# Performance work log

Measured on AMD Instinct MI355X. Metric: run time of the kernel, lower is better.

Reference implementation:

```python
import jax, jax.numpy as jnp
import numpy as np


def _get_pairs(top_k_centers):
    """Returns (p0, p1) int32 arrays of shape [B, S]: for each object a, the
    IoU-best partner a', ordered so the larger-L1 box comes first (as in source)."""
    cx, cy, h, w = jnp.split(top_k_centers, 4, axis=-1)  # [B,S,1] each, cxcyhw
    box = jnp.concatenate([cx - 0.5 * w, cy - 0.5 * h, cx + 0.5 * w, cy + 0.5 * h], axis=-1)  # [B,S,4] xyxy
    S = box.shape[1]
    b1 = box[:, :, None, :]  # [B,S,1,4]
    b2 = box[:, None, :, :]  # [B,1,S,4]
    inter_mins = jnp.maximum(b1[..., :2], b2[..., :2])
    inter_maxs = jnp.maximum(b1[..., 2:], b2[..., 2:])  # NOTE: source uses maximum here (kept faithful)
    inter_wh = jnp.clip(inter_maxs - inter_mins, 0.0)
    inter_area = inter_wh[..., 0] * inter_wh[..., 1]  # [B,S,S]
    area = (box[..., 2] - box[..., 0]) * (box[..., 3] - box[..., 1])  # [B,S]
    union = area[:, :, None] + area[:, None, :] - inter_area
    iou = inter_area / union - jnp.eye(S, dtype=inter_area.dtype)
    partner = jnp.argmax(iou, axis=-1)  # [B,S] int
    self_idx = jnp.broadcast_to(jnp.arange(S), partner.shape)
    l1 = jnp.abs(box[..., 2] - box[..., 0]) + jnp.abs(box[..., 3] - box[..., 1])  # [B,S]
    l1_partner = jnp.take_along_axis(l1, partner, axis=-1)
    keep = l1 >= l1_partner  # larger-L1 element goes first
    p0 = jnp.where(keep, self_idx, partner)
    p1 = jnp.where(keep, partner, self_idx)
    return p0, p1


def _gather_pair(a2, p):
    # a2: [B,H,S,S]; p: [B,S]. out[b,h,a,c] = a2[b,h,p[b,a],p[b,c]]
    rows = jnp.take_along_axis(a2, p[:, None, :, None], axis=2)
    return jnp.take_along_axis(rows, p[:, None, None, :], axis=3)


def setup_inputs() -> dict:
    key = jax.random.key(0)
    kq, kk, kv, kc = jax.random.split(key, 4)
    B, H, S, D = 8, 8, 1024, 64
    return {
        "query": jax.random.normal(kq, (B, H, S, D), dtype=jnp.float32),
        "key": jax.random.normal(kk, (B, H, S, D), dtype=jnp.float32),
        "value": jax.random.normal(kv, (B, H, S, D), dtype=jnp.float32),
        "top_k_centers": jax.random.uniform(kc, (B, S, 4), dtype=jnp.float32),
    }


def reference(query, key, value, top_k_centers):
    B, H, S, D = query.shape
    p0, p1 = _get_pairs(top_k_centers)
    # A2(a,b) = <q_{pi_a}, k_{pi_b}> + <q_{pi_a'}, k_{pi_b'}>
    a2 = jnp.einsum('bhqd,bhkd->bhqk', query, key)  # [B,H,S,S]
    scores = (_gather_pair(a2, p0) + _gather_pair(a2, p1)) * (1.0 / np.sqrt(2.0 * D))
    attn = jax.nn.softmax(scores, axis=-1)
    o2 = jnp.einsum('bhqk,bhkd->bhqd', attn, value)  # [B,H,S,D]
    return o2.transpose(0, 2, 1, 3).reshape(B, S, H * D)
```

## Files before the change

### kernel.cpp

```cpp
#include <hip/hip_runtime.h>
#include <hip/hip_bf16.h>

#define B_ 8
#define H_ 8
#define S_ 1024
#define D_ 64
#define KT 32
#define NSTEP 16

typedef float f32x16 __attribute__((ext_vector_type(16)));
typedef short s16x8 __attribute__((ext_vector_type(8)));
typedef unsigned int u32;

#define CSCALE ((float)(1.4426950408889634 / 11.313708498984761))

static __device__ __forceinline__ unsigned short f2bf(float f) {
    union { float f; unsigned u; } v; v.f = f;
    unsigned r = v.u + 0x7FFF + ((v.u >> 16) & 1);
    return (unsigned short)(r >> 16);
}

static __device__ __forceinline__ u32 cvtpk(float lo, float hi) {
    u32 r;
    asm("v_cvt_pk_bf16_f32 %0, %1, %2" : "=v"(r) : "v"(lo), "v"(hi));
    return r;
}

static __device__ __forceinline__ void glds16(const void* g, void* l) {
    __builtin_amdgcn_global_load_lds(
        (const __attribute__((address_space(1))) unsigned int*)(uintptr_t)g,
        (__attribute__((address_space(3))) unsigned int*)(unsigned)(uintptr_t)l,
        16, 0, 0);
}

__global__ __launch_bounds__(256) void pairs_kernel(const float* __restrict__ centers,
                                                    int* __restrict__ p0,
                                                    int* __restrict__ p1) {
#pragma clang fp contract(off)
    __shared__ __align__(16) float4 box4[S_];
    __shared__ float areas[S_], l1s[S_];
    const int b = blockIdx.y;
    const int t = threadIdx.x;
    for (int idx = t; idx < S_; idx += 256) {
        const float4 c = *reinterpret_cast<const float4*>(centers + ((size_t)b * S_ + idx) * 4);
        const float cx = c.x, cy = c.y, hh = c.z, ww = c.w;
        const float x0 = cx - 0.5f * ww;
        const float y0 = cy - 0.5f * hh;
        const float x1 = cx + 0.5f * ww;
        const float y1 = cy + 0.5f * hh;
        box4[idx] = float4{x0, y0, x1, y1};
        areas[idx] = (x1 - x0) * (y1 - y0);
        l1s[idx] = fabsf(x1 - x0) + fabsf(y1 - y0);
    }
    __syncthreads();
    const int i = blockIdx.x * 16 + (t >> 4);
    const int c16 = t & 15;
    const float4 bi = box4[i];
    const float ai = areas[i];
    float best = -1e38f; int arg = 0;
    #pragma unroll 4
    for (int it = 0; it < 64; ++it) {
        const int j = it * 16 + c16;
        const float4 bj = box4[j];
        const float aj = areas[j];
        float wx = fmaxf(bi.z, bj.z) - fmaxf(bi.x, bj.x);
        float wy = fmaxf(bi.w, bj.w) - fmaxf(bi.y, bj.y);
        wx = fmaxf(wx, 0.0f);
        wy = fmaxf(wy, 0.0f);
        const float inter = wx * wy;
        const float uni = (ai + aj) - inter;
        float v = inter / uni;
        if (j == i) v = v - 1.0f;
        if (v > best) { best = v; arg = j; }
    }
    #pragma unroll
    for (int m = 1; m <= 8; m <<= 1) {
        const float ob = __shfl_xor(best, m);
        const int oa = __shfl_xor(arg, m);
        if (ob > best || (ob == best && oa < arg)) { best = ob; arg = oa; }
    }
    if (c16 == 0) {
        const int partner = arg;
        const float l1i = l1s[i], l1p = l1s[partner];
        const int keep = (l1i >= l1p) ? 1 : 0;
        p0[b * S_ + i] = keep ? i : partner;
        p1[b * S_ + i] = keep ? partner : i;
    }
}

__global__ __launch_bounds__(256) void prep_kv(const float* __restrict__ k,
                                               const float* __restrict__ v,
                                               const int* __restrict__ p0,
                                               const int* __restrict__ p1,
                                               unsigned short* __restrict__ Kg,
                                               unsigned short* __restrict__ Vt) {
    __shared__ float tile[64][65];
    const int gid = blockIdx.x;
    const int grp = (gid >> 3) & 15;
    const int bh = ((gid >> 7) << 3) | (gid & 7);
    const int b = bh >> 3;
    const int s0 = grp * 64;
    const int kt0 = grp * 2;
    const int t = threadIdx.x;
    {
        const float* kp = k + (size_t)bh * S_ * D_;
        const int* p0b = p0 + b * S_;
        const int* p1b = p1 + b * S_;
        unsigned short* KgB = Kg + (size_t)bh * 131072;
        for (int it = 0; it < 4; ++it) {
            const int flat = it * 256 + t;
            const int ktl = flat >> 9;
            const int L = (flat >> 6) & 7;
            const int lane = flat & 63;
            const int s = s0 + ktl * 32 + (lane & 31);
            const int c = (L << 1) + (lane >> 5);
            const int i0 = p0b[s], i1 = p1b[s];
            const float* src = (c < 8) ? (kp + (size_t)i0 * D_ + c * 8)
                                       : (kp + (size_t)i1 * D_ + (c - 8) * 8);
            const float4 f0 = *reinterpret_cast<const float4*>(src);
            const float4 f1 = *reinterpret_cast<const float4*>(src + 4);
            union { u32 u[4]; s16x8 v; } pk;
            pk.u[0] = cvtpk(f0.x, f0.y);
            pk.u[1] = cvtpk(f0.z, f0.w);
            pk.u[2] = cvtpk(f1.x, f1.y);
            pk.u[3] = cvtpk(f1.z, f1.w);
            *reinterpret_cast<s16x8*>(KgB + ((size_t)((kt0 + ktl) * 8 + L) * 64 + lane) * 8) = pk.v;
        }
    }
    {
        const float* vp = v + ((size_t)bh * S_ + s0) * D_;
        const int row = t >> 2, cpart = (t & 3) * 16;
        for (int jj = 0; jj < 4; ++jj) {
            const float4 x = *reinterpret_cast<const float4*>(&vp[(size_t)row * D_ + cpart + jj * 4]);
            tile[row][cpart + jj * 4 + 0] = x.x;
            tile[row][cpart + jj * 4 + 1] = x.y;
            tile[row][cpart + jj * 4 + 2] = x.z;
            tile[row][cpart + jj * 4 + 3] = x.w;
        }
        __syncthreads();
        unsigned short* VtB = Vt + (size_t)bh * 65536;
        for (int it = 0; it < 2; ++it) {
            const int flat = it * 256 + t;
            const int ktl = flat >> 8;
            const int L = (flat >> 6) & 3;
            const int lane = flat & 63;
            const int dt = L >> 1, ks = L & 1;
            const int d = dt * 32 + (lane & 31);
            const int sr = ktl * 32 + ks * 16 + ((lane >> 5) << 3);
            unsigned short hh[8];
            #pragma unroll
            for (int e = 0; e < 8; ++e) hh[e] = f2bf(tile[sr + e][d]);
            *reinterpret_cast<s16x8*>(VtB + ((size_t)((kt0 + ktl) * 4 + L) * 64 + lane) * 8) =
                *reinterpret_cast<s16x8*>(hh);
        }
    }
}

__global__ __launch_bounds__(256, 4) void attn_kernel(const float* __restrict__ q,
                                                      const unsigned short* __restrict__ Kg,
                                                      const unsigned short* __restrict__ Vt,
                                                      const int* __restrict__ p0,
                                                      const int* __restrict__ p1,
                                                      float* __restrict__ out) {
    __shared__ __align__(16) char smem[40960];
    auto Osh = reinterpret_cast<float(*)[32][66]>(smem);
    auto lsh = reinterpret_cast<float(*)[32]>(smem + 33792);

    const int tid = threadIdx.x;
    const int w = tid >> 6;
    const int r = w >> 1;
    const int s = w & 1;
    const int lane = tid & 63;
    const int qc = lane & 31;
    const int hi = lane >> 5;
    const int gid = blockIdx.x;
    const int rowtile = (gid >> 3) & 15;
    const int bh = ((gid >> 7) << 3) | (gid & 7);
    const int b = bh >> 3;
    const int h = bh & 7;

    const float* qp = q + (size_t)bh * S_ * D_;
    const unsigned short* KgB = Kg + (size_t)bh * 131072;
    const unsigned short* VtB = Vt + (size_t)bh * 65536;

    char* const strbase = smem + s * 20480;

    auto STAGE_K = [&](int t, int buf) {
        const int kt = s * NSTEP + t;
        char* base = strbase + buf * 8192;
        #pragma unroll
        for (int j = 0; j < 4; ++j) {
            const int L = r * 4 + j;
            glds16(KgB + ((size_t)(kt * 8 + L) * 64 + lane) * 8, base + L * 1024);
        }
    };
    auto STAGE_V = [&](int t) {
        const int kt = s * NSTEP + t;
        #pragma unroll
        for (int L = 0; L < 4; ++L)
            glds16(VtB + ((size_t)(kt * 4 + L) * 64 + lane) * 8, strbase + 16384 + L * 1024);
    };

    STAGE_K(0, 0);

    s16x8 qf[8];
    {
        const int qr = rowtile * 64 + r * 32 + qc;
        const int i0 = p0[b * S_ + qr], i1 = p1[b * S_ + qr];
        #pragma unroll
        for (int p = 0; p < 8; ++p) {
            const int k0 = 16 * p + 8 * hi;
            const float* src = (p < 4) ? (qp + (size_t)i0 * D_ + k0)
                                       : (qp + (size_t)i1 * D_ + (k0 - 64));
            const float4 f0 = *reinterpret_cast<const float4*>(src);
            const float4 f1 = *reinterpret_cast<const float4*>(src + 4);
            union { u32 u[4]; s16x8 v; } pk;
            pk.u[0] = cvtpk(f0.x * CSCALE, f0.y * CSCALE);
            pk.u[1] = cvtpk(f0.z * CSCALE, f0.w * CSCALE);
            pk.u[2] = cvtpk(f1.x * CSCALE, f1.y * CSCALE);
            pk.u[3] = cvtpk(f1.z * CSCALE, f1.w * CSCALE);
            qf[p] = pk.v;
        }
    }
    __syncthreads();

    f32x16 oacc0 = {}, oacc1 = {};
    f32x16 lsum = {};

    for (int t = 0; t < NSTEP; ++t) {
        const int buf = t & 1;
        STAGE_V(t);
        if (t + 1 < NSTEP) STAGE_K(t + 1, buf ^ 1);

        const unsigned short* KsT = reinterpret_cast<const unsigned short*>(strbase + buf * 8192);
        const unsigned short* VsT = reinterpret_cast<const unsigned short*>(strbase + 16384);

        f32x16 st = {};
        #pragma unroll
        for (int L = 0; L < 8; ++L) {
            const s16x8 kf = *reinterpret_cast<const s16x8*>(KsT + L * 512 + lane * 8);
            st = __builtin_amdgcn_mfma_f32_32x32x16_bf16(kf, qf[L], st, 0, 0, 0);
        }

        #pragma unroll
        for (int i = 0; i < 16; ++i) st[i] = exp2f(st[i]);
        lsum += st;

        u32 U[8];
        #pragma unroll
        for (int i = 0; i < 8; ++i) U[i] = cvtpk(st[2 * i], st[2 * i + 1]);

        if (t + 1 < NSTEP) asm volatile("s_waitcnt vmcnt(4)" ::: "memory");
        else               asm volatile("s_waitcnt vmcnt(0)" ::: "memory");
        __builtin_amdgcn_sched_barrier(0);

        #pragma unroll
        for (int ks = 0; ks < 2; ++ks) {
            const int a = 4 * ks;
            const u32 sendA = hi ? U[a] : U[a + 2];
            const u32 recvA = __shfl_xor(sendA, 32);
            const u32 w0 = hi ? recvA : U[a];
            const u32 w2 = hi ? U[a + 2] : recvA;
            const u32 sendB = hi ? U[a + 1] : U[a + 3];
            const u32 recvB = __shfl_xor(sendB, 32);
            const u32 w1 = hi ? recvB : U[a + 1];
            const u32 w3 = hi ? U[a + 3] : recvB;
            union { u32 u[4]; s16x8 v; } pf;
            pf.u[0] = w0; pf.u[1] = w1; pf.u[2] = w2; pf.u[3] = w3;
            const s16x8 vf0 = *reinterpret_cast<const s16x8*>(VsT + ks * 512 + lane * 8);
            oacc0 = __builtin_amdgcn_mfma_f32_32x32x16_bf16(vf0, pf.v, oacc0, 0, 0, 0);
            const s16x8 vf1 = *reinterpret_cast<const s16x8*>(VsT + (2 + ks) * 512 + lane * 8);
            oacc1 = __builtin_amdgcn_mfma_f32_32x32x16_bf16(vf1, pf.v, oacc1, 0, 0, 0);
        }
        __syncthreads();
    }

    float l_run;
    {
        float a8[8];
        #pragma unroll
        for (int i = 0; i < 8; ++i) a8[i] = lsum[i] + lsum[i + 8];
        #pragma unroll
        for (int i = 0; i < 4; ++i) a8[i] += a8[i + 4];
        l_run = (a8[0] + a8[1]) + (a8[2] + a8[3]);
        l_run += __shfl_xor(l_run, 32);
    }

    #pragma unroll
    for (int i = 0; i < 16; ++i) {
        const int d0 = (i & 3) + 8 * (i >> 2) + 4 * hi;
        Osh[w][qc][d0] = oacc0[i];
        Osh[w][qc][32 + d0] = oacc1[i];
    }
    if (hi == 0) lsh[w][qc] = l_run;
    __syncthreads();

    const int row = tid >> 2;
    const int rr = row >> 5;
    const int lrow = row & 31;
    const int dc = (tid & 3) * 16;
    const int wa = rr * 2, wb = rr * 2 + 1;
    const float den = lsh[wa][lrow] + lsh[wb][lrow];
    const float inv = 1.0f / den;
    const int qrg = rowtile * 64 + row;
    float* orow = out + ((size_t)b * S_ + qrg) * (H_ * D_) + h * D_ + dc;
    #pragma unroll
    for (int e4 = 0; e4 < 4; ++e4) {
        float4 o;
        o.x = (Osh[wa][lrow][dc + e4 * 4 + 0] + Osh[wb][lrow][dc + e4 * 4 + 0]) * inv;
        o.y = (Osh[wa][lrow][dc + e4 * 4 + 1] + Osh[wb][lrow][dc + e4 * 4 + 1]) * inv;
        o.z = (Osh[wa][lrow][dc + e4 * 4 + 2] + Osh[wb][lrow][dc + e4 * 4 + 2]) * inv;
        o.w = (Osh[wa][lrow][dc + e4 * 4 + 3] + Osh[wb][lrow][dc + e4 * 4 + 3]) * inv;
        *reinterpret_cast<float4*>(orow + e4 * 4) = o;
    }
}

extern "C" void kernel_launch(void* const* d_in, const int* in_sizes, int n_in,
                              void* d_out, int out_size, void* d_ws, size_t ws_size,
                              hipStream_t stream) {
    (void)in_sizes; (void)n_in; (void)out_size; (void)ws_size;
    const float* q = (const float*)d_in[0];
    const float* k = (const float*)d_in[1];
    const float* v = (const float*)d_in[2];
    const float* c = (const float*)d_in[3];
    float* out = (float*)d_out;
    int* p0 = (int*)d_ws;
    int* p1 = p0 + B_ * S_;
    unsigned short* Kg = (unsigned short*)((char*)d_ws + 65536);
    unsigned short* Vt = Kg + (size_t)B_ * H_ * S_ * 128;
    pairs_kernel<<<dim3(64, 8), 256, 0, stream>>>(c, p0, p1);
    prep_kv<<<dim3(1024), 256, 0, stream>>>(k, v, p0, p1, Kg, Vt);
    attn_kernel<<<dim3(1024), 256, 0, stream>>>(q, Kg, Vt, p0, p1, out);
}
```

Baseline: 72.84 us.

## Load V fragments directly to registers, split QK MFMA chains, use permlane32 swap

V tiles are now loaded straight from global memory into registers per lane instead of being staged through LDS, which shrinks shared memory and drops the explicit vmcnt wait. The QK^T MFMA chain is split into two independent accumulators that are summed afterward, shortening the dependency chain. The cross-half-wave exchange of P fragments replaces ds shuffles with v_permlane32_swap_b32. The risk is that V global-load latency is exposed, since there is no explicit prefetch and the compiler-inserted waits may stall before the PV MFMAs.

```diff
diff --git a/kernel.cpp b/kernel.cpp
--- a/kernel.cpp
+++ b/kernel.cpp
@@ -162,7 +162,7 @@
                                                       const int* __restrict__ p0,
                                                       const int* __restrict__ p1,
                                                       float* __restrict__ out) {
-    __shared__ __align__(16) char smem[40960];
+    __shared__ __align__(16) char smem[34304];
     auto Osh = reinterpret_cast<float(*)[32][66]>(smem);
     auto lsh = reinterpret_cast<float(*)[32]>(smem + 33792);
 
@@ -181,9 +181,9 @@
 
     const float* qp = q + (size_t)bh * S_ * D_;
     const unsigned short* KgB = Kg + (size_t)bh * 131072;
-    const unsigned short* VtB = Vt + (size_t)bh * 65536;
-
-    char* const strbase = smem + s * 20480;
+    const unsigned short* VtL = Vt + (size_t)bh * 65536 + (size_t)lane * 8;
+
+    char* const strbase = smem + s * 16384;
 
     auto STAGE_K = [&](int t, int buf) {
         const int kt = s * NSTEP + t;
@@ -193,12 +193,6 @@
             const int L = r * 4 + j;
             glds16(KgB + ((size_t)(kt * 8 + L) * 64 + lane) * 8, base + L * 1024);
         }
-    };
-    auto STAGE_V = [&](int t) {
-        const int kt = s * NSTEP + t;
-        #pragma unroll
-        for (int L = 0; L < 4; ++L)
-            glds16(VtB + ((size_t)(kt * 4 + L) * 64 + lane) * 8, strbase + 16384 + L * 1024);
     };
 
     STAGE_K(0, 0);
@@ -229,18 +223,26 @@
 
     for (int t = 0; t < NSTEP; ++t) {
         const int buf = t & 1;
-        STAGE_V(t);
+        const int kt = s * NSTEP + t;
+
+        s16x8 vf[4];
+        #pragma unroll
+        for (int L = 0; L < 4; ++L)
+            vf[L] = *reinterpret_cast<const s16x8*>(VtL + (size_t)(kt * 4 + L) * 512);
+
         if (t + 1 < NSTEP) STAGE_K(t + 1, buf ^ 1);
 
         const unsigned short* KsT = reinterpret_cast<const unsigned short*>(strbase + buf * 8192);
-        const unsigned short* VsT = reinterpret_cast<const unsigned short*>(strbase + 16384);
-
-        f32x16 st = {};
-        #pragma unroll
-        for (int L = 0; L < 8; ++L) {
-            const s16x8 kf = *reinterpret_cast<const s16x8*>(KsT + L * 512 + lane * 8);
-            st = __builtin_amdgcn_mfma_f32_32x32x16_bf16(kf, qf[L], st, 0, 0, 0);
-        }
+
+        f32x16 sa = {}, sb = {};
+        #pragma unroll
+        for (int L = 0; L < 4; ++L) {
+            const s16x8 kfa = *reinterpret_cast<const s16x8*>(KsT + L * 512 + lane * 8);
+            sa = __builtin_amdgcn_mfma_f32_32x32x16_bf16(kfa, qf[L], sa, 0, 0, 0);
+            const s16x8 kfb = *reinterpret_cast<const s16x8*>(KsT + (4 + L) * 512 + lane * 8);
+            sb = __builtin_amdgcn_mfma_f32_32x32x16_bf16(kfb, qf[4 + L], sb, 0, 0, 0);
+        }
+        f32x16 st = sa + sb;
 
         #pragma unroll
         for (int i = 0; i < 16; ++i) st[i] = exp2f(st[i]);
@@ -250,27 +252,17 @@
         #pragma unroll
         for (int i = 0; i < 8; ++i) U[i] = cvtpk(st[2 * i], st[2 * i + 1]);
 
-        if (t + 1 < NSTEP) asm volatile("s_waitcnt vmcnt(4)" ::: "memory");
-        else               asm volatile("s_waitcnt vmcnt(0)" ::: "memory");
-        __builtin_amdgcn_sched_barrier(0);
-
         #pragma unroll
         for (int ks = 0; ks < 2; ++ks) {
             const int a = 4 * ks;
-            const u32 sendA = hi ? U[a] : U[a + 2];
-            const u32 recvA = __shfl_xor(sendA, 32);
-            const u32 w0 = hi ? recvA : U[a];
-            const u32 w2 = hi ? U[a + 2] : recvA;
-            const u32 sendB = hi ? U[a + 1] : U[a + 3];
-            const u32 recvB = __shfl_xor(sendB, 32);
-            const u32 w1 = hi ? recvB : U[a + 1];
-            const u32 w3 = hi ? U[a + 3] : recvB;
+            u32 w0 = U[a], w2 = U[a + 2];
+            u32 w1 = U[a + 1], w3 = U[a + 3];
+            asm("v_permlane32_swap_b32 %0, %1" : "+v"(w0), "+v"(w2));
+            asm("v_permlane32_swap_b32 %0, %1" : "+v"(w1), "+v"(w3));
             union { u32 u[4]; s16x8 v; } pf;
             pf.u[0] = w0; pf.u[1] = w1; pf.u[2] = w2; pf.u[3] = w3;
-            const s16x8 vf0 = *reinterpret_cast<const s16x8*>(VsT + ks * 512 + lane * 8);
-            oacc0 = __builtin_amdgcn_mfma_f32_32x32x16_bf16(vf0, pf.v, oacc0, 0, 0, 0);
-            const s16x8 vf1 = *reinterpret_cast<const s16x8*>(VsT + (2 + ks) * 512 + lane * 8);
-            oacc1 = __builtin_amdgcn_mfma_f32_32x32x16_bf16(vf1, pf.v, oacc1, 0, 0, 0);
+            oacc0 = __builtin_amdgcn_mfma_f32_32x32x16_bf16(vf[ks], pf.v, oacc0, 0, 0, 0);
+            oacc1 = __builtin_amdgcn_mfma_f32_32x32x16_bf16(vf[2 + ks], pf.v, oacc1, 0, 0, 0);
         }
         __syncthreads();
     }
```

Result: slower. 78.73 us (+8.1%).
